# Optimization experiments

Hardware: AMD Instinct MI355X
Metric: run time of the kernel (lower is better)

Reference implementation:

```python
import jax, jax.numpy as jnp
import numpy as np
from jax import lax

B, C, H, W = 2, 256, 64, 64
KC, RD = C // 8, C // 16  # key_channels=32, GatherExcite rd_channels=16
EPS = 1e-5


def setup_inputs() -> dict:
    key = jax.random.key(0)
    ks = jax.random.split(key, 17)
    s = 0.05
    n = lambda k, shp: jax.random.normal(k, shp, jnp.float32) * s
    return {
        "x": jax.random.normal(ks[0], (B, C, H, W), jnp.float32),
        "Wq": n(ks[1], (KC, C)),
        "Wk": n(ks[2], (KC, C)),
        "Wv": n(ks[3], (C, C)),
        "Wb1": n(ks[4], (KC, C)),
        "Wb2": n(ks[5], (KC, C)),
        "w_gb": jax.random.normal(ks[6], (), jnp.float32),  # 1x1 conv on 1-channel bias map
        "ge_w1": n(ks[7], (RD, C)),
        "ge_b1": jnp.zeros((RD,), jnp.float32),
        "ge_w2": n(ks[8], (C, RD)),
        "ge_b2": jnp.zeros((C,), jnp.float32),
        "Wo": n(ks[9], (C, C)),
        "bn_scale": jnp.ones((C,), jnp.float32),
        "bn_bias": jnp.zeros((C,), jnp.float32),
        "bn_mean": jax.random.normal(ks[10], (C,), jnp.float32) * 0.01,
        "bn_var": jnp.ones((C,), jnp.float32),
        "gamma": jax.random.normal(ks[11], (), jnp.float32) * 0.1,
    }


def _conv1x1(t, w):  # t: [B,Cin,H,W], w: [Cout,Cin]
    return jnp.einsum('bchw,oc->bohw', t, w)


def reference(x, Wq, Wk, Wv, Wb1, Wb2, w_gb, ge_w1, ge_b1, ge_w2, ge_b2,
              Wo, bn_scale, bn_bias, bn_mean, bn_var, gamma):
    b, c, h, w = x.shape
    hw = h * w

    # GatherExcite (extent=0, use_mlp=True, gate=sigmoid): global mean -> ConvMlp -> sigmoid gate
    m = x.mean(axis=(2, 3), keepdims=True)                     # [B,C,1,1]
    g = jax.nn.relu(_conv1x1(m, ge_w1) + ge_b1[None, :, None, None])
    g = _conv1x1(g, ge_w2) + ge_b2[None, :, None, None]
    key_in = x * jax.nn.sigmoid(g)                             # [B,C,H,W]

    value = _conv1x1(x, Wv).reshape(b, c, hw).transpose(0, 2, 1)   # [B,HW,C]
    query = _conv1x1(x, Wq).reshape(b, KC, hw).transpose(0, 2, 1)  # [B,HW,Kc]
    key_f = _conv1x1(key_in, Wk).reshape(b, KC, hw)                # [B,Kc,HW]

    sim = jnp.einsum('bnk,bkm->bnm', query, key_f)                 # [B,HW,HW]

    # bias branch (dropout is identity at eval)
    b1 = jax.nn.relu(_conv1x1(x, Wb1)).reshape(b, KC, hw)          # [B,Kc,HW]
    b2 = jax.nn.relu(_conv1x1(x, Wb2)).reshape(b, KC, hw)          # [B,Kc,HW]
    bias = jnp.einsum('bkn,bkm->bnm', b1, b2)                      # [B,HW,HW]

    # AvgPool2d(k=3, s=1, pad=1, count_include_pad=True) on [B,1,HW,HW]
    pooled = lax.reduce_window(bias[:, None], 0.0, lax.add,
                               (1, 1, 3, 3), (1, 1, 1, 1),
                               [(0, 0), (0, 0), (1, 1), (1, 1)]) / 9.0
    bias_map = jax.nn.sigmoid(w_gb * pooled)[:, 0]                 # [B,HW,HW]

    attn = jax.nn.softmax(sim * bias_map, axis=-1)                 # [B,HW,HW]
    ctx = jnp.einsum('bnm,bmc->bnc', attn, value)                  # [B,HW,C]
    ctx = ctx.transpose(0, 2, 1).reshape(b, c, h, w)

    # W: conv1x1 -> BatchNorm (inference) -> ReLU
    y = _conv1x1(ctx, Wo)
    y = (y - bn_mean[None, :, None, None]) * (bn_scale / jnp.sqrt(bn_var + EPS))[None, :, None, None] \
        + bn_bias[None, :, None, None]
    y = jax.nn.relu(y)

    return gamma * y + x
```

## Files before the change

kernel.cpp:

```cpp
#include <hip/hip_runtime.h>
#include <hip/hip_bf16.h>

typedef __bf16 bf16;
typedef __bf16 v8bf __attribute__((ext_vector_type(8)));
typedef __bf16 v4bf __attribute__((ext_vector_type(4)));
typedef float v4f __attribute__((ext_vector_type(4)));

#define HW 4096
#define CH 256
#define KC 32
#define RD 16
#define NB 2
#define BNEPS 1e-5f
#define VSTRIDE 4224
#define LOG2E 1.4426950408889634f

__device__ __forceinline__ float fexp2(float x) {
#if __has_builtin(__builtin_amdgcn_exp2f)
  return __builtin_amdgcn_exp2f(x);
#else
  return exp2f(x);
#endif
}
__device__ __forceinline__ float frcp(float x) {
#if __has_builtin(__builtin_amdgcn_rcpf)
  return __builtin_amdgcn_rcpf(x);
#else
  return 1.f / x;
#endif
}

__device__ __forceinline__ int xcd_swz(int bid, int nwg) {
  return (bid & 7) * (nwg >> 3) + (bid >> 3);
}

#define OFF_QT     0u
#define OFF_KT     524288u
#define OFF_BS1    1048576u
#define OFF_BS2    1572864u
#define OFF_VT     2097152u
#define OFF_B1R    6422528u
#define OFF_B2R    6946816u
#define OFF_PACC   7471104u
#define OFF_PL     41025536u
#define OFF_WOBF   41287680u
#define OFF_XBT    41418752u
#define OFF_WALL   45613056u
#define OFF_MPART  46006272u

__global__ __launch_bounds__(256) void k_prep(const float* __restrict__ x,
    bf16* __restrict__ xbt, float* __restrict__ mpart) {
  __shared__ __align__(16) float ts[64][68];
  const int blk = blockIdx.x;
  const int b  = blk >> 8;
  const int id = blk & 255;
  const int ct = id >> 6, nt = id & 63;
  const int c0 = ct * 64, n0 = nt * 64;
  const int t = threadIdx.x;
  const int crow = t >> 2, nch = (t & 3) * 16;
  const float* xp = x + ((size_t)(b * CH + c0 + crow)) * HW + n0 + nch;
  #pragma unroll
  for (int i = 0; i < 4; ++i)
    *(v4f*)&ts[crow][nch + i * 4] = *(const v4f*)(xp + i * 4);
  __syncthreads();
  {
    float p = 0.f;
    #pragma unroll
    for (int j = 0; j < 16; ++j) p += ts[crow][nch + j];
    p += __shfl_xor(p, 1);
    p += __shfl_xor(p, 2);
    if ((t & 3) == 0) mpart[(size_t)(b * CH + c0 + crow) * 64 + nt] = p;
  }
  const int nl = t >> 2, cc0 = (t & 3) * 16;
  bf16* dst = xbt + ((size_t)(b * HW + n0 + nl)) * CH + c0 + cc0;
  v8bf o0, o1;
  #pragma unroll
  for (int j = 0; j < 8; ++j) { o0[j] = (bf16)ts[cc0 + j][nl]; o1[j] = (bf16)ts[cc0 + 8 + j][nl]; }
  *(v8bf*)dst = o0;
  *(v8bf*)(dst + 8) = o1;
}

__global__ __launch_bounds__(256) void k_pack(
    const float* __restrict__ mpart,
    const float* __restrict__ gw1, const float* __restrict__ gb1,
    const float* __restrict__ gw2, const float* __restrict__ gb2,
    const float* __restrict__ Wq, const float* __restrict__ Wk,
    const float* __restrict__ Wb1, const float* __restrict__ Wb2,
    const float* __restrict__ Wv, const float* __restrict__ Wo,
    bf16* __restrict__ wall, bf16* __restrict__ wo_bf) {
  __shared__ float ms[CH];
  __shared__ float hid[RD];
  const int blk = blockIdx.x;
  const int t = threadIdx.x;
  if (blk >= 768) {
    int i = (blk - 768) * 256 + t;
    wo_bf[i] = (bf16)Wo[i];
    return;
  }
  const int b = blk / 384, row = blk % 384;
  float v;
  if (row < 32)       v = Wq[row * CH + t] * LOG2E;
  else if (row < 64) {
    float m = 0.f;
    const float* mp = mpart + (size_t)(b * CH + t) * 64;
    #pragma unroll
    for (int j = 0; j < 64; ++j) m += mp[j];
    ms[t] = m * (1.0f / HW);
    __syncthreads();
    if (t < RD) {
      float a = gb1[t];
      for (int c = 0; c < CH; ++c) a += gw1[t * CH + c] * ms[c];
      hid[t] = fmaxf(a, 0.f);
    }
    __syncthreads();
    float a = gb2[t];
    #pragma unroll
    for (int r = 0; r < RD; ++r) a += gw2[t * RD + r] * hid[r];
    float s = 1.f / (1.f + __expf(-a));
    v = Wk[(row - 32) * CH + t] * s;
  }
  else if (row < 96)  v = Wb1[(row - 64) * CH + t];
  else if (row < 128) v = Wb2[(row - 96) * CH + t];
  else                v = Wv[(row - 128) * CH + t];
  wall[((size_t)b * 384 + row) * CH + t] = (bf16)v;
}

__global__ __launch_bounds__(256, 4) void k_proj(
    const bf16* __restrict__ xbt, const bf16* __restrict__ wall,
    bf16* __restrict__ qt, bf16* __restrict__ kt,
    bf16* __restrict__ b1r, bf16* __restrict__ b2r, bf16* __restrict__ vt) {
  __shared__ __align__(16) bf16 xs[32][264];
  __shared__ __align__(16) bf16 tr[4][16][24];
  const int blk = blockIdx.x;
  const int b  = blk >> 9;
  const int bm = (blk >> 7) & 3;
  const int nt = blk & 127;
  const int n0 = nt * 32;
  const int t = threadIdx.x;
  {
    const int row = t >> 3, c0 = (t & 7) * 32;
    const bf16* src = xbt + ((size_t)(b * HW + n0 + row)) * CH + c0;
    #pragma unroll
    for (int i = 0; i < 4; ++i)
      *(v8bf*)&xs[row][c0 + i * 8] = *(const v8bf*)(src + i * 8);
  }
  __syncthreads();
  const int w = t >> 6, lane = t & 63, cl = lane & 15, kh = lane >> 4;
  const int nsub = (w & 1) * 16;
  const int otrio = (w >> 1) * 3;
  const v4f vzero = {0.f, 0.f, 0.f, 0.f};
  v4f acc[3] = {vzero, vzero, vzero};
  const bf16* wb = wall + ((size_t)b * 384 + bm * 96) * CH;
  for (int kk = 0; kk < 8; ++kk) {
    v8bf bx = *(const v8bf*)&xs[nsub + cl][kk * 32 + kh * 8];
    #pragma unroll
    for (int j = 0; j < 3; ++j) {
      v8bf af = *(const v8bf*)(wb + (size_t)((otrio + j) * 16 + cl) * CH + kk * 32 + kh * 8);
      acc[j] = __builtin_amdgcn_mfma_f32_16x16x32_bf16(af, bx, acc[j], 0, 0, 0);
    }
  }
  const int n = n0 + nsub + cl;
  #pragma unroll
  for (int j = 0; j < 3; ++j) {
    const int o0 = bm * 96 + (otrio + j) * 16;
    if (o0 < 128) {
      const bool rel = (o0 >= 64);
      v4bf pk;
      #pragma unroll
      for (int r = 0; r < 4; ++r) {
        float v = acc[j][r];
        if (rel) v = fmaxf(v, 0.f);
        pk[r] = (bf16)v;
      }
      const int seg = o0 >> 5;
      bf16* base = seg == 0 ? qt : seg == 1 ? kt : seg == 2 ? b1r : b2r;
      *(v4bf*)&base[((size_t)b * HW + n) * KC + (o0 & 31) + kh * 4] = pk;
    } else {
      #pragma unroll
      for (int r = 0; r < 4; ++r) tr[w][kh * 4 + r][cl] = (bf16)acc[j][r];
      asm volatile("s_waitcnt lgkmcnt(0)" ::: "memory");
      __builtin_amdgcn_sched_barrier(0);
      const int row = lane >> 2, nch = (lane & 3) * 4;
      v4bf d = *(const v4bf*)&tr[w][row][nch];
      *(v4bf*)&vt[((size_t)b * CH + (o0 - 128) + row) * VSTRIDE + n0 + nsub + nch] = d;
    }
  }
}

__global__ __launch_bounds__(256) void k_pool(const bf16* __restrict__ b1r,
    const bf16* __restrict__ b2r, const float* __restrict__ wgb,
    bf16* __restrict__ bs1, bf16* __restrict__ bs2) {
  int i = blockIdx.x * 256 + threadIdx.x;
  int n = (i >> 5) & (HW - 1);
  float a = (float)b1r[i], c = (float)b2r[i];
  if (n > 0)      { a += (float)b1r[i - KC]; c += (float)b2r[i - KC]; }
  if (n < HW - 1) { a += (float)b1r[i + KC]; c += (float)b2r[i + KC]; }
  const float ws = -LOG2E * wgb[0] * (1.f / 9.f);
  bs1[i] = (bf16)(a * ws);
  bs2[i] = (bf16)c;
}

__global__ __launch_bounds__(256, 4) void k_attn(
    const bf16* __restrict__ qtg, const bf16* __restrict__ ktg,
    const bf16* __restrict__ bs1g, const bf16* __restrict__ bs2g,
    const bf16* __restrict__ vtg,
    bf16* __restrict__ pacc, float* __restrict__ pl) {
  __shared__ __align__(16) bf16 vbuf[128][64];
  __shared__ __align__(16) bf16 kbuf[2][32][40];
  __shared__ __align__(16) bf16 bbuf[2][32][40];
  __shared__ __align__(16) bf16 plds[2][64][40];
  const int blk = xcd_swz(blockIdx.x, 1024);
  const int rt  = blk >> 3;
  const int os  = blk & 7;
  const int b   = rt >> 6;
  const int row0 = (rt & 63) * 64;
  const int t = threadIdx.x;
  const int w = t >> 6;
  const int lane = t & 63;
  const int cl = lane & 15, kh = lane >> 4;
  const int kb = os * 512;
  const v4f vzero = {0.f, 0.f, 0.f, 0.f};
  const size_t qoff = ((size_t)(b * HW + row0 + w * 16 + cl)) * KC + kh * 8;
  const v8bf qf  = *(const v8bf*)(qtg + qoff);
  const v8bf b1f = *(const v8bf*)(bs1g + qoff);
  const bf16* kt = ktg + (size_t)b * HW * KC;
  const bf16* b2 = bs2g + (size_t)b * HW * KC;
  const bf16* vt = vtg + (size_t)b * CH * VSTRIDE;
  const int sr = (t >> 2) & 31, sl = (t & 3) * 8;
  const bf16* sbase = (t < 128) ? kt : b2;
  bf16* sd0 = (t < 128) ? &kbuf[0][sr][sl] : &bbuf[0][sr][sl];
  bf16* sd1 = (t < 128) ? &kbuf[1][sr][sl] : &bbuf[1][sr][sl];
  const int vsl = lane & 3;
  const int vslot3 = ((((lane >> 2) & 1) * 4 + vsl) ^ (lane >> 3)) * 8;
  const int rline = w * 32 + (cl >> 1);
  const int rslot = ((((cl & 1) * 4) + kh) ^ (cl >> 1)) * 8;

  *(v8bf*)sd0 = *(const v8bf*)(sbase + (size_t)(kb + sr) * KC + sl);
  __syncthreads();

  v4f acc[16];
  #pragma unroll
  for (int f = 0; f < 16; ++f) acc[f] = vzero;
  float psum = 0.f;

  for (int s = 0; s < 16; ++s) {
    const int m0 = kb + s * 32;
    const int pb = s & 1;
    v8bf vr[4];
    #pragma unroll
    for (int i = 0; i < 4; ++i)
      vr[i] = *(const v8bf*)(vt + (size_t)(w * 64 + i * 16 + (lane >> 2)) * VSTRIDE + m0 + vsl * 8);
    v8bf pr;
    if (s < 15)
      pr = *(const v8bf*)(sbase + (size_t)(m0 + 32 + sr) * KC + sl);
    #pragma unroll
    for (int cb = 0; cb < 2; ++cb) {
      v8bf kf  = *(const v8bf*)&kbuf[pb][cb * 16 + cl][kh * 8];
      v8bf b2f = *(const v8bf*)&bbuf[pb][cb * 16 + cl][kh * 8];
      v4f sim = __builtin_amdgcn_mfma_f32_16x16x32_bf16(kf,  qf,  vzero, 0, 0, 0);
      v4f bia = __builtin_amdgcn_mfma_f32_16x16x32_bf16(b2f, b1f, vzero, 0, 0, 0);
      v4bf pk;
      #pragma unroll
      for (int r = 0; r < 4; ++r) {
        float bm = frcp(1.f + fexp2(bia[r]));
        float pv = fexp2(sim[r] * bm);
        psum += pv;
        pk[r] = (bf16)pv;
      }
      *(v4bf*)&plds[pb][w * 16 + cl][cb * 16 + kh * 4] = pk;
    }
    #pragma unroll
    for (int i = 0; i < 4; ++i)
      *(v8bf*)&vbuf[w * 32 + i * 8 + (lane >> 3)][vslot3] = vr[i];
    if (s < 15) {
      bf16* sd = pb ? sd0 : sd1;
      *(v8bf*)sd = pr;
    }
    __syncthreads();
    v8bf vf[4], pa[4];
    #pragma unroll
    for (int f = 0; f < 4; ++f)
      vf[f] = *(const v8bf*)&vbuf[rline + f * 8][rslot];
    #pragma unroll
    for (int rg = 0; rg < 4; ++rg)
      pa[rg] = *(const v8bf*)&plds[pb][rg * 16 + cl][kh * 8];
    #pragma unroll
    for (int rg = 0; rg < 4; ++rg)
      #pragma unroll
      for (int f = 0; f < 4; ++f)
        acc[rg * 4 + f] = __builtin_amdgcn_mfma_f32_16x16x32_bf16(pa[rg], vf[f], acc[rg * 4 + f], 0, 0, 0);
  }
  __syncthreads();

  {
    float s2 = psum;
    s2 += __shfl_xor(s2, 16);
    s2 += __shfl_xor(s2, 32);
    if (kh == 0) pl[blk * 64 + w * 16 + cl] = s2;
  }
  bf16 (*ep)[64] = (bf16 (*)[64])vbuf;
  bf16* po = pacc + (size_t)blk * 64 * CH;
  for (int rg = 0; rg < 4; ++rg) {
    #pragma unroll
    for (int f = 0; f < 4; ++f)
      #pragma unroll
      for (int r = 0; r < 4; ++r)
        ep[w * 16 + kh * 4 + r][f * 16 + cl] = (bf16)acc[rg * 4 + f][r];
    asm volatile("s_waitcnt lgkmcnt(0)" ::: "memory");
    __builtin_amdgcn_sched_barrier(0);
    #pragma unroll
    for (int it = 0; it < 2; ++it) {
      int row = lane >> 2, chunk = it * 4 + (lane & 3);
      v8bf d = *(const v8bf*)&ep[w * 16 + row][chunk * 8];
      *(v8bf*)&po[(size_t)(rg * 16 + row) * CH + w * 64 + chunk * 8] = d;
    }
  }
}

__global__ __launch_bounds__(256) void k_outc(
    const bf16* __restrict__ pacc, const float* __restrict__ pl,
    const bf16* __restrict__ wo,
    const float* __restrict__ bns, const float* __restrict__ bnb,
    const float* __restrict__ bnm, const float* __restrict__ bnv,
    const float* __restrict__ gamma, const float* __restrict__ x,
    float* __restrict__ out) {
  __shared__ __align__(16) bf16 cs[16][264];
  const int blk = xcd_swz(blockIdx.x, 512);
  const int n0g = blk * 16;
  const int b   = n0g >> 12;
  const int n0  = n0g & (HW - 1);
  const int t = threadIdx.x;
  const int base = (blk >> 2) * 8;
  {
    const int r16 = t >> 4;
    const int ch0 = (t & 15) * 16;
    const int rl = (blk & 3) * 16 + r16;
    float den = 0.f;
    #pragma unroll
    for (int s = 0; s < 8; ++s) den += pl[(base + s) * 64 + rl];
    const float inv = 1.f / den;
    float sum[16];
    #pragma unroll
    for (int j = 0; j < 16; ++j) sum[j] = 0.f;
    #pragma unroll
    for (int s = 0; s < 8; ++s) {
      const bf16* pp = &pacc[((size_t)(base + s) * 64 + rl) * CH + ch0];
      v8bf p0 = *(const v8bf*)pp;
      v8bf p1 = *(const v8bf*)(pp + 8);
      #pragma unroll
      for (int j = 0; j < 8; ++j) { sum[j] += (float)p0[j]; sum[8 + j] += (float)p1[j]; }
    }
    v8bf o0, o1;
    #pragma unroll
    for (int j = 0; j < 8; ++j) {
      o0[j] = (bf16)(sum[j] * inv);
      o1[j] = (bf16)(sum[8 + j] * inv);
    }
    *(v8bf*)&cs[r16][ch0] = o0;
    *(v8bf*)&cs[r16][ch0 + 8] = o1;
  }
  __syncthreads();
  const int w = t >> 6, lane = t & 63, cl = lane & 15, kh = lane >> 4;
  const v4f vzero = {0.f, 0.f, 0.f, 0.f};
  v8bf a[8];
  #pragma unroll
  for (int kk = 0; kk < 8; ++kk)
    a[kk] = *(const v8bf*)&cs[cl][kk * 32 + kh * 8];
  v4f acc[4] = {vzero, vzero, vzero, vzero};
  #pragma unroll
  for (int kk = 0; kk < 8; ++kk)
    #pragma unroll
    for (int cg = 0; cg < 4; ++cg) {
      v8bf bfr = *(const v8bf*)(wo + (size_t)(w * 64 + cg * 16 + cl) * CH + kk * 32 + kh * 8);
      acc[cg] = __builtin_amdgcn_mfma_f32_16x16x32_bf16(a[kk], bfr, acc[cg], 0, 0, 0);
    }
  const float g = gamma[0];
  #pragma unroll
  for (int cg = 0; cg < 4; ++cg) {
    int o = w * 64 + cg * 16 + cl;
    float isc = bns[o] / sqrtf(bnv[o] + BNEPS);
    float mu = bnm[o], bb = bnb[o];
    size_t oi = ((size_t)b * CH + o) * HW + n0 + kh * 4;
    v4f xv = *(const v4f*)&x[oi];
    v4f ov;
    #pragma unroll
    for (int r = 0; r < 4; ++r) {
      float v = (acc[cg][r] - mu) * isc + bb;
      v = fmaxf(v, 0.f);
      ov[r] = g * v + xv[r];
    }
    *(v4f*)&out[oi] = ov;
  }
}

extern "C" void kernel_launch(void* const* d_in, const int* in_sizes, int n_in,
                              void* d_out, int out_size, void* d_ws, size_t ws_size,
                              hipStream_t stream) {
  const float* x    = (const float*)d_in[0];
  const float* Wq   = (const float*)d_in[1];
  const float* Wk   = (const float*)d_in[2];
  const float* Wv   = (const float*)d_in[3];
  const float* Wb1  = (const float*)d_in[4];
  const float* Wb2  = (const float*)d_in[5];
  const float* wgb  = (const float*)d_in[6];
  const float* gw1  = (const float*)d_in[7];
  const float* gb1  = (const float*)d_in[8];
  const float* gw2  = (const float*)d_in[9];
  const float* gb2  = (const float*)d_in[10];
  const float* Wo   = (const float*)d_in[11];
  const float* bns  = (const float*)d_in[12];
  const float* bnb  = (const float*)d_in[13];
  const float* bnm  = (const float*)d_in[14];
  const float* bnv  = (const float*)d_in[15];
  const float* gam  = (const float*)d_in[16];

  char* ws = (char*)d_ws;
  bf16* qt    = (bf16*)(ws + OFF_QT);
  bf16* kt    = (bf16*)(ws + OFF_KT);
  bf16* bs1   = (bf16*)(ws + OFF_BS1);
  bf16* bs2   = (bf16*)(ws + OFF_BS2);
  bf16* vt    = (bf16*)(ws + OFF_VT);
  bf16* b1r   = (bf16*)(ws + OFF_B1R);
  bf16* b2r   = (bf16*)(ws + OFF_B2R);
  bf16* pacc  = (bf16*)(ws + OFF_PACC);
  float* plv  = (float*)(ws + OFF_PL);
  bf16* wobf  = (bf16*)(ws + OFF_WOBF);
  bf16* xbt   = (bf16*)(ws + OFF_XBT);
  bf16* wall  = (bf16*)(ws + OFF_WALL);
  float* mprt = (float*)(ws + OFF_MPART);
  float* out  = (float*)d_out;

  hipLaunchKernelGGL(k_prep, dim3(512),  dim3(256), 0, stream, x, xbt, mprt);
  hipLaunchKernelGGL(k_pack, dim3(1024), dim3(256), 0, stream, mprt, gw1, gb1, gw2, gb2,
                     Wq, Wk, Wb1, Wb2, Wv, Wo, wall, wobf);
  hipLaunchKernelGGL(k_proj, dim3(1024), dim3(256), 0, stream, xbt, wall, qt, kt, b1r, b2r, vt);
  hipLaunchKernelGGL(k_pool, dim3(NB * HW * KC / 256), dim3(256), 0, stream, b1r, b2r, wgb, bs1, bs2);
  hipLaunchKernelGGL(k_attn, dim3(1024), dim3(256), 0, stream, qt, kt, bs1, bs2, vt, pacc, plv);
  hipLaunchKernelGGL(k_outc, dim3(512),  dim3(256), 0, stream, pacc, plv, wobf, bns, bnb, bnm, bnv, gam, x, out);
}
```

Baseline: 85.49 us.

## Store V pre-swizzled in MFMA fragment layout and load directly in attention

The projection kernel now writes the value tensor directly in the per-lane MFMA B-operand fragment order, in place of a padded transposed layout. The attention kernel therefore loads V fragments straight from global memory into registers, dropping the LDS staging buffer, its swizzled stores and its reads. The projection kernel is also retiled to 16 positions per block, with each wave computing 96 output rows, which halves its grid. The trade is less LDS traffic and footprint in attention against global V loads that now sit right after the barrier, with no software prefetch to hide their latency.

After: 80.73 us. -5.6%, faster.

```diff
diff --git a/kernel.cpp b/kernel.cpp
--- a/kernel.cpp
+++ b/kernel.cpp
@@ -12,7 +12,6 @@
 #define RD 16
 #define NB 2
 #define BNEPS 1e-5f
-#define VSTRIDE 4224
 #define LOG2E 1.4426950408889634f
 
 __device__ __forceinline__ float fexp2(float x) {
@@ -38,15 +37,15 @@
 #define OFF_KT     524288u
 #define OFF_BS1    1048576u
 #define OFF_BS2    1572864u
-#define OFF_VT     2097152u
-#define OFF_B1R    6422528u
-#define OFF_B2R    6946816u
-#define OFF_PACC   7471104u
-#define OFF_PL     41025536u
-#define OFF_WOBF   41287680u
-#define OFF_XBT    41418752u
-#define OFF_WALL   45613056u
-#define OFF_MPART  46006272u
+#define OFF_VF     2097152u
+#define OFF_B1R    6291456u
+#define OFF_B2R    6815744u
+#define OFF_PACC   7340032u
+#define OFF_PL     40894464u
+#define OFF_WOBF   41156608u
+#define OFF_XBT    41287680u
+#define OFF_WALL   45481984u
+#define OFF_MPART  45875200u
 
 __global__ __launch_bounds__(256) void k_prep(const float* __restrict__ x,
     bf16* __restrict__ xbt, float* __restrict__ mpart) {
@@ -128,41 +127,36 @@
 __global__ __launch_bounds__(256, 4) void k_proj(
     const bf16* __restrict__ xbt, const bf16* __restrict__ wall,
     bf16* __restrict__ qt, bf16* __restrict__ kt,
-    bf16* __restrict__ b1r, bf16* __restrict__ b2r, bf16* __restrict__ vt) {
-  __shared__ __align__(16) bf16 xs[32][264];
+    bf16* __restrict__ b1r, bf16* __restrict__ b2r, bf16* __restrict__ vfg) {
+  __shared__ __align__(16) bf16 xs[16][264];
   __shared__ __align__(16) bf16 tr[4][16][24];
   const int blk = blockIdx.x;
-  const int b  = blk >> 9;
-  const int bm = (blk >> 7) & 3;
-  const int nt = blk & 127;
-  const int n0 = nt * 32;
+  const int b = blk >> 8, nt = blk & 255;
+  const int n0 = nt * 16;
   const int t = threadIdx.x;
   {
-    const int row = t >> 3, c0 = (t & 7) * 32;
+    const int row = t >> 4, c0 = (t & 15) * 16;
     const bf16* src = xbt + ((size_t)(b * HW + n0 + row)) * CH + c0;
-    #pragma unroll
-    for (int i = 0; i < 4; ++i)
-      *(v8bf*)&xs[row][c0 + i * 8] = *(const v8bf*)(src + i * 8);
+    *(v8bf*)&xs[row][c0] = *(const v8bf*)src;
+    *(v8bf*)&xs[row][c0 + 8] = *(const v8bf*)(src + 8);
   }
   __syncthreads();
   const int w = t >> 6, lane = t & 63, cl = lane & 15, kh = lane >> 4;
-  const int nsub = (w & 1) * 16;
-  const int otrio = (w >> 1) * 3;
   const v4f vzero = {0.f, 0.f, 0.f, 0.f};
-  v4f acc[3] = {vzero, vzero, vzero};
-  const bf16* wb = wall + ((size_t)b * 384 + bm * 96) * CH;
+  v4f acc[6] = {vzero, vzero, vzero, vzero, vzero, vzero};
+  const bf16* wb = wall + ((size_t)b * 384 + w * 96) * CH;
   for (int kk = 0; kk < 8; ++kk) {
-    v8bf bx = *(const v8bf*)&xs[nsub + cl][kk * 32 + kh * 8];
-    #pragma unroll
-    for (int j = 0; j < 3; ++j) {
-      v8bf af = *(const v8bf*)(wb + (size_t)((otrio + j) * 16 + cl) * CH + kk * 32 + kh * 8);
+    v8bf bx = *(const v8bf*)&xs[cl][kk * 32 + kh * 8];
+    #pragma unroll
+    for (int j = 0; j < 6; ++j) {
+      v8bf af = *(const v8bf*)(wb + (size_t)(j * 16 + cl) * CH + kk * 32 + kh * 8);
       acc[j] = __builtin_amdgcn_mfma_f32_16x16x32_bf16(af, bx, acc[j], 0, 0, 0);
     }
   }
-  const int n = n0 + nsub + cl;
-  #pragma unroll
-  for (int j = 0; j < 3; ++j) {
-    const int o0 = bm * 96 + (otrio + j) * 16;
+  const int n = n0 + cl;
+  #pragma unroll
+  for (int j = 0; j < 6; ++j) {
+    const int o0 = w * 96 + j * 16;
     if (o0 < 128) {
       const bool rel = (o0 >= 64);
       v4bf pk;
@@ -180,9 +174,13 @@
       for (int r = 0; r < 4; ++r) tr[w][kh * 4 + r][cl] = (bf16)acc[j][r];
       asm volatile("s_waitcnt lgkmcnt(0)" ::: "memory");
       __builtin_amdgcn_sched_barrier(0);
-      const int row = lane >> 2, nch = (lane & 3) * 4;
-      v4bf d = *(const v4bf*)&tr[w][row][nch];
-      *(v4bf*)&vt[((size_t)b * CH + (o0 - 128) + row) * VSTRIDE + n0 + nsub + nch] = d;
+      if (lane < 32) {
+        const int clf = lane & 15, khl = (lane >> 4) & 1;
+        const int khf = (((n0 >> 4) & 1) << 1) + khl;
+        const int s = n0 >> 5, f = (o0 - 128) >> 4;
+        v8bf d = *(const v8bf*)&tr[w][clf][khl * 8];
+        *(v8bf*)&vfg[((((size_t)b * 128 + s) * 16 + f) * 64 + khf * 16 + clf) * 8] = d;
+      }
     }
   }
 }
@@ -203,12 +201,12 @@
 __global__ __launch_bounds__(256, 4) void k_attn(
     const bf16* __restrict__ qtg, const bf16* __restrict__ ktg,
     const bf16* __restrict__ bs1g, const bf16* __restrict__ bs2g,
-    const bf16* __restrict__ vtg,
+    const bf16* __restrict__ vfg,
     bf16* __restrict__ pacc, float* __restrict__ pl) {
-  __shared__ __align__(16) bf16 vbuf[128][64];
   __shared__ __align__(16) bf16 kbuf[2][32][40];
   __shared__ __align__(16) bf16 bbuf[2][32][40];
   __shared__ __align__(16) bf16 plds[2][64][40];
+  __shared__ __align__(16) bf16 escr[4][16][72];
   const int blk = xcd_swz(blockIdx.x, 1024);
   const int rt  = blk >> 3;
   const int os  = blk & 7;
@@ -225,15 +223,11 @@
   const v8bf b1f = *(const v8bf*)(bs1g + qoff);
   const bf16* kt = ktg + (size_t)b * HW * KC;
   const bf16* b2 = bs2g + (size_t)b * HW * KC;
-  const bf16* vt = vtg + (size_t)b * CH * VSTRIDE;
+  const bf16* vfb = vfg + ((((size_t)b * 128 + (kb >> 5)) * 16) + w * 4) * 512 + (size_t)lane * 8;
   const int sr = (t >> 2) & 31, sl = (t & 3) * 8;
   const bf16* sbase = (t < 128) ? kt : b2;
   bf16* sd0 = (t < 128) ? &kbuf[0][sr][sl] : &bbuf[0][sr][sl];
   bf16* sd1 = (t < 128) ? &kbuf[1][sr][sl] : &bbuf[1][sr][sl];
-  const int vsl = lane & 3;
-  const int vslot3 = ((((lane >> 2) & 1) * 4 + vsl) ^ (lane >> 3)) * 8;
-  const int rline = w * 32 + (cl >> 1);
-  const int rslot = ((((cl & 1) * 4) + kh) ^ (cl >> 1)) * 8;
 
   *(v8bf*)sd0 = *(const v8bf*)(sbase + (size_t)(kb + sr) * KC + sl);
   __syncthreads();
@@ -246,10 +240,6 @@
   for (int s = 0; s < 16; ++s) {
     const int m0 = kb + s * 32;
     const int pb = s & 1;
-    v8bf vr[4];
-    #pragma unroll
-    for (int i = 0; i < 4; ++i)
-      vr[i] = *(const v8bf*)(vt + (size_t)(w * 64 + i * 16 + (lane >> 2)) * VSTRIDE + m0 + vsl * 8);
     v8bf pr;
     if (s < 15)
       pr = *(const v8bf*)(sbase + (size_t)(m0 + 32 + sr) * KC + sl);
@@ -269,26 +259,24 @@
       }
       *(v4bf*)&plds[pb][w * 16 + cl][cb * 16 + kh * 4] = pk;
     }
-    #pragma unroll
-    for (int i = 0; i < 4; ++i)
-      *(v8bf*)&vbuf[w * 32 + i * 8 + (lane >> 3)][vslot3] = vr[i];
     if (s < 15) {
       bf16* sd = pb ? sd0 : sd1;
       *(v8bf*)sd = pr;
     }
     __syncthreads();
-    v8bf vf[4], pa[4];
-    #pragma unroll
-    for (int f = 0; f < 4; ++f)
-      vf[f] = *(const v8bf*)&vbuf[rline + f * 8][rslot];
-    #pragma unroll
-    for (int rg = 0; rg < 4; ++rg)
-      pa[rg] = *(const v8bf*)&plds[pb][rg * 16 + cl][kh * 8];
-    #pragma unroll
-    for (int rg = 0; rg < 4; ++rg)
-      #pragma unroll
-      for (int f = 0; f < 4; ++f)
-        acc[rg * 4 + f] = __builtin_amdgcn_mfma_f32_16x16x32_bf16(pa[rg], vf[f], acc[rg * 4 + f], 0, 0, 0);
+    const bf16* vs = vfb + (size_t)s * 8192;
+    v8bf vf0 = *(const v8bf*)(vs);
+    v8bf vf1 = *(const v8bf*)(vs + 512);
+    v8bf vf2 = *(const v8bf*)(vs + 1024);
+    v8bf vf3 = *(const v8bf*)(vs + 1536);
+    #pragma unroll
+    for (int rg = 0; rg < 4; ++rg) {
+      v8bf pa = *(const v8bf*)&plds[pb][rg * 16 + cl][kh * 8];
+      acc[rg * 4 + 0] = __builtin_amdgcn_mfma_f32_16x16x32_bf16(pa, vf0, acc[rg * 4 + 0], 0, 0, 0);
+      acc[rg * 4 + 1] = __builtin_amdgcn_mfma_f32_16x16x32_bf16(pa, vf1, acc[rg * 4 + 1], 0, 0, 0);
+      acc[rg * 4 + 2] = __builtin_amdgcn_mfma_f32_16x16x32_bf16(pa, vf2, acc[rg * 4 + 2], 0, 0, 0);
+      acc[rg * 4 + 3] = __builtin_amdgcn_mfma_f32_16x16x32_bf16(pa, vf3, acc[rg * 4 + 3], 0, 0, 0);
+    }
   }
   __syncthreads();
 
@@ -298,20 +286,19 @@
     s2 += __shfl_xor(s2, 32);
     if (kh == 0) pl[blk * 64 + w * 16 + cl] = s2;
   }
-  bf16 (*ep)[64] = (bf16 (*)[64])vbuf;
   bf16* po = pacc + (size_t)blk * 64 * CH;
   for (int rg = 0; rg < 4; ++rg) {
     #pragma unroll
     for (int f = 0; f < 4; ++f)
       #pragma unroll
       for (int r = 0; r < 4; ++r)
-        ep[w * 16 + kh * 4 + r][f * 16 + cl] = (bf16)acc[rg * 4 + f][r];
+        escr[w][kh * 4 + r][f * 16 + cl] = (bf16)acc[rg * 4 + f][r];
     asm volatile("s_waitcnt lgkmcnt(0)" ::: "memory");
     __builtin_amdgcn_sched_barrier(0);
     #pragma unroll
     for (int it = 0; it < 2; ++it) {
       int row = lane >> 2, chunk = it * 4 + (lane & 3);
-      v8bf d = *(const v8bf*)&ep[w * 16 + row][chunk * 8];
+      v8bf d = *(const v8bf*)&escr[w][row][chunk * 8];
       *(v8bf*)&po[(size_t)(rg * 16 + row) * CH + w * 64 + chunk * 8] = d;
     }
   }
@@ -419,7 +406,7 @@
   bf16* kt    = (bf16*)(ws + OFF_KT);
   bf16* bs1   = (bf16*)(ws + OFF_BS1);
   bf16* bs2   = (bf16*)(ws + OFF_BS2);
-  bf16* vt    = (bf16*)(ws + OFF_VT);
+  bf16* vfg   = (bf16*)(ws + OFF_VF);
   bf16* b1r   = (bf16*)(ws + OFF_B1R);
   bf16* b2r   = (bf16*)(ws + OFF_B2R);
   bf16* pacc  = (bf16*)(ws + OFF_PACC);
@@ -433,8 +420,8 @@
   hipLaunchKernelGGL(k_prep, dim3(512),  dim3(256), 0, stream, x, xbt, mprt);
   hipLaunchKernelGGL(k_pack, dim3(1024), dim3(256), 0, stream, mprt, gw1, gb1, gw2, gb2,
                      Wq, Wk, Wb1, Wb2, Wv, Wo, wall, wobf);
-  hipLaunchKernelGGL(k_proj, dim3(1024), dim3(256), 0, stream, xbt, wall, qt, kt, b1r, b2r, vt);
+  hipLaunchKernelGGL(k_proj, dim3(512),  dim3(256), 0, stream, xbt, wall, qt, kt, b1r, b2r, vfg);
   hipLaunchKernelGGL(k_pool, dim3(NB * HW * KC / 256), dim3(256), 0, stream, b1r, b2r, wgb, bs1, bs2);
-  hipLaunchKernelGGL(k_attn, dim3(1024), dim3(256), 0, stream, qt, kt, bs1, bs2, vt, pacc, plv);
+  hipLaunchKernelGGL(k_attn, dim3(1024), dim3(256), 0, stream, qt, kt, bs1, bs2, vfg, pacc, plv);
   hipLaunchKernelGGL(k_outc, dim3(512),  dim3(256), 0, stream, pacc, plv, wobf, bns, bnb, bnm, bnv, gam, x, out);
 }
```
